# Performance work log

Measured on AMD Instinct MI355X. Metric: run time of the kernel, lower is better.

Reference implementation:

```python
import jax, jax.numpy as jnp
import numpy as np

B, D, N, M, R, C = 512, 16, 64, 32, 32, 10  # batch, divisions, feat_in, feat_map, TR-rank, categories


def setup_inputs() -> dict:
    key = jax.random.key(0)
    k1, k2, k3, k4 = jax.random.split(key, 4)
    tensor = jax.random.normal(k1, (B, D, N), dtype=jnp.float32)
    W_fm = jax.random.normal(k2, (N, M), dtype=jnp.float32) / np.sqrt(N)
    b_fm = jax.random.normal(k3, (M,), dtype=jnp.float32) * 0.01
    # one [R, M, R] tensor-ring core per (category, division)
    G = jax.random.normal(k4, (C, D, R, M, R), dtype=jnp.float32) / np.sqrt(M * R)
    return {"tensor": tensor, "W_fm": W_fm, "b_fm": b_fm, "G": G}


def reference(tensor, W_fm, b_fm, G):
    # FeatureMap: learned linear n -> m applied per division  [B, D, M]
    feat = jnp.einsum('bdn,nm->bdm', tensor, W_fm) + b_fm
    # CoreKernelTensorRing per (category, division): [B,M] x [R,M,R] -> [B,R,R]
    cores = jnp.einsum('bdm,cdimj->cdbij', feat, G)  # [C, D, B, R, R]
    # __foward_products: chained batched matmul along divisions (structural loop, D fixed)
    prod = cores[:, 0]  # [C, B, R, R]
    for d in range(1, D):
        prod = jnp.matmul(prod, cores[:, d])
    # __calculate_traces: per-sample trace, one logit per category
    logits = jnp.einsum('cbii->bc', prod)  # [B, C]
    return jax.nn.log_softmax(logits, axis=1)
```

## Files before the change

kernel.cpp:

```cpp
#include <hip/hip_runtime.h>
#include <math.h>

#define BB 512
#define DD 16
#define NN 64
#define MM 32
#define RR 32
#define CC 10
#define BBLK 16
#define SS 2
#define DSEG (DD / SS)
#define ROWH 40
#define BREGH 1304

typedef _Float16 v8h __attribute__((ext_vector_type(8)));
typedef float v4f __attribute__((ext_vector_type(4)));

union H8 { unsigned int u[4]; v8h h; _Float16 e[8]; };
union H4 { unsigned int u[2]; _Float16 e[4]; };

__device__ __forceinline__ unsigned int split_pack(float x) {
    _Float16 h = (_Float16)x;
    _Float16 l = (_Float16)(x - (float)h);
    unsigned int hb = (unsigned int)__builtin_bit_cast(unsigned short, h);
    unsigned int lb = (unsigned int)__builtin_bit_cast(unsigned short, l);
    return (hb << 16) | lb;
}

__device__ __forceinline__ float unpackf(unsigned int u) {
    _Float16 h = __builtin_bit_cast(_Float16, (unsigned short)(u >> 16));
    _Float16 l = __builtin_bit_cast(_Float16, (unsigned short)(u & 0xffffu));
    return (float)h + (float)l;
}

__global__ void produce_kernel(const float* __restrict__ tensor,
                               const float* __restrict__ W,
                               const float* __restrict__ bias,
                               const float* __restrict__ G,
                               _Float16* __restrict__ fh,
                               _Float16* __restrict__ gh) {
    if (blockIdx.x < 1024) {
        int t  = blockIdx.x * 256 + threadIdx.x;
        int m  = t & (MM - 1);
        int bd = t >> 5;
        const float* tp = tensor + bd * NN;
        float acc = bias[m];
#pragma unroll
        for (int n = 0; n < NN; ++n) acc += tp[n] * W[n * MM + m];
        fh[t] = (_Float16)acc;
    } else {
        int gid  = (blockIdx.x - 1024) * 256 + threadIdx.x;
        int l    = gid & 63;
        int tile = (gid >> 6) & 63;
        int d    = (gid >> 12) & 15;
        int c    = gid >> 16;
        int i    = tile >> 1;
        int jj   = 16 * (tile & 1) + (l & 15);
        int q    = l >> 4;
        const float* src = G + ((((size_t)c * DD + d) * RR + i) * MM + 8 * q) * RR + jj;
        H8 v;
#pragma unroll
        for (int r = 0; r < 8; ++r)
            v.e[r] = (_Float16)src[(size_t)r * RR];
        *(v8h*)(gh + (size_t)gid * 8) = v.h;
    }
}

__global__ __launch_bounds__(512, 6) void chain_kernel(
    const _Float16* __restrict__ feat_h,
    const _Float16* __restrict__ g_h,
    unsigned int* __restrict__ segP)
{
    __shared__ __align__(16) _Float16 lds[BBLK * BREGH];

    const int bid  = blockIdx.x;
    const int c    = bid >> 6;
    const int rem  = bid & 63;
    const int s    = rem & 1;
    const int b0   = (rem >> 1) * BBLK;
    const int d0   = s * DSEG;
    const int t    = threadIdx.x;
    const int w    = t >> 6;
    const int lane = t & 63;
    const int q    = lane >> 4;
    const int j4   = lane & 15;

    v8h pah[2][2];

    for (int dd = 0; dd < DSEG; ++dd) {
        const int d = d0 + dd;
        __syncthreads();
        {
            const size_t fo = (size_t)(b0 + j4) * (DD * MM) + d * MM + q * 8;
            v8h afh = *(const v8h*)(feat_h + fo);
            const size_t gbase = (size_t)(c * DD + d) * 32768;
#pragma unroll
            for (int jh = 0; jh < 2; ++jh) {
                v4f av[4];
#pragma unroll
                for (int ii = 0; ii < 4; ++ii) {
                    const int tile = w * 8 + 2 * ii + jh;
                    v8h g = *(const v8h*)(g_h + gbase + ((size_t)tile * 64 + lane) * 8);
                    v4f z = {0.f, 0.f, 0.f, 0.f};
                    av[ii] = __builtin_amdgcn_mfma_f32_16x16x32_f16(afh, g, z, 0, 0, 0);
                }
#pragma unroll
                for (int reg = 0; reg < 4; ++reg) {
                    H4 hv;
                    hv.e[0] = (_Float16)av[0][reg];
                    hv.e[1] = (_Float16)av[1][reg];
                    hv.e[2] = (_Float16)av[2][reg];
                    hv.e[3] = (_Float16)av[3][reg];
                    *reinterpret_cast<uint2*>(
                        &lds[(4 * q + reg) * BREGH + (16 * jh + j4) * ROWH + 4 * w]) =
                        make_uint2(hv.u[0], hv.u[1]);
                }
            }
        }
        __syncthreads();
#pragma unroll
        for (int cc = 0; cc < 2; ++cc) {
            const int b = 2 * w + cc;
            _Float16* base = lds + b * BREGH;
            if (dd == 0) {
#pragma unroll
                for (int mi = 0; mi < 2; ++mi) {
                    H8 a;
#pragma unroll
                    for (int r = 0; r < 8; ++r)
                        a.e[r] = base[(8 * q + r) * ROWH + 16 * mi + j4];
                    pah[cc][mi] = a.h;
                }
            } else {
                v8h bf[2];
#pragma unroll
                for (int ni = 0; ni < 2; ++ni)
                    bf[ni] = *(const v8h*)(base + (16 * ni + j4) * ROWH + 8 * q);
                v4f acc[2][2];
#pragma unroll
                for (int mi = 0; mi < 2; ++mi)
#pragma unroll
                    for (int ni = 0; ni < 2; ++ni) {
                        v4f z = {0.f, 0.f, 0.f, 0.f};
                        acc[mi][ni] = __builtin_amdgcn_mfma_f32_16x16x32_f16(
                            pah[cc][mi], bf[ni], z, 0, 0, 0);
                    }
                if (dd < DSEG - 1) {
#pragma unroll
                    for (int mi = 0; mi < 2; ++mi)
#pragma unroll
                        for (int ni = 0; ni < 2; ++ni)
#pragma unroll
                            for (int reg = 0; reg < 4; ++reg)
                                base[(16 * mi + 4 * q + reg) * ROWH + 16 * ni + j4] =
                                    (_Float16)acc[mi][ni][reg];
                    __builtin_amdgcn_sched_barrier(0);
#pragma unroll
                    for (int mi = 0; mi < 2; ++mi)
                        pah[cc][mi] = *(const v8h*)(base + (16 * mi + j4) * ROWH + 8 * q);
                } else {
                    unsigned int* dst = segP +
                        ((size_t)(c * BB + (b0 + b)) * SS + s) * 1024;
#pragma unroll
                    for (int mi = 0; mi < 2; ++mi)
#pragma unroll
                        for (int ni = 0; ni < 2; ++ni)
#pragma unroll
                            for (int reg = 0; reg < 4; ++reg)
                                dst[(16 * mi + 4 * q + reg) * 32 + 16 * ni + j4] =
                                    split_pack(acc[mi][ni][reg]);
                }
            }
        }
    }
}

__global__ __launch_bounds__(256) void combine_lsm_kernel(
    const unsigned int* __restrict__ segP,
    float* __restrict__ out)
{
    const int t    = threadIdx.x;
    const int b    = blockIdx.x * 4 + (t >> 6);
    const int lane = t & 63;
    const int i    = lane & 31;
    const int hf   = lane >> 5;

    float tr[CC];
#pragma unroll
    for (int c = 0; c < CC; ++c) {
        const unsigned int* P0 = segP + ((size_t)(c * BB + b) * SS + 0) * 1024;
        const unsigned int* P1 = P0 + 1024;
        const uint4* r0 = (const uint4*)(P0 + i * 32 + hf * 16);
        float acc = 0.f;
#pragma unroll
        for (int v = 0; v < 4; ++v) {
            uint4 x = r0[v];
            unsigned int us[4] = {x.x, x.y, x.z, x.w};
#pragma unroll
            for (int e = 0; e < 4; ++e) {
                int l = hf * 16 + v * 4 + e;
                acc += unpackf(us[e]) * unpackf(P1[l * 32 + i]);
            }
        }
        tr[c] = acc;
    }
#pragma unroll
    for (int c = 0; c < CC; ++c) {
#pragma unroll
        for (int off = 32; off > 0; off >>= 1)
            tr[c] += __shfl_down(tr[c], off);
    }
    if (lane == 0) {
        float mx = -1e30f;
#pragma unroll
        for (int c = 0; c < CC; ++c) mx = fmaxf(mx, tr[c]);
        float ssum = 0.f;
#pragma unroll
        for (int c = 0; c < CC; ++c) ssum += expf(tr[c] - mx);
        float ls = logf(ssum);
#pragma unroll
        for (int c = 0; c < CC; ++c) out[b * CC + c] = tr[c] - mx - ls;
    }
}

extern "C" void kernel_launch(void* const* d_in, const int* in_sizes, int n_in,
                              void* d_out, int out_size, void* d_ws, size_t ws_size,
                              hipStream_t stream) {
    const float* tensor = (const float*)d_in[0];
    const float* W      = (const float*)d_in[1];
    const float* bias   = (const float*)d_in[2];
    const float* G      = (const float*)d_in[3];
    float* out = (float*)d_out;

    const size_t FEAT = (size_t)BB * DD * MM;
    const size_t GPK  = (size_t)CC * DD * 64 * 64 * 8;
    _Float16* fh = (_Float16*)d_ws;
    _Float16* gh = fh + FEAT;
    unsigned int* segP = (unsigned int*)(gh + GPK);

    produce_kernel<<<1024 + (int)(GPK / 8 / 256), 256, 0, stream>>>(
        tensor, W, bias, G, fh, gh);
    chain_kernel<<<CC * (BB / BBLK) * SS, 512, 0, stream>>>(fh, gh, segP);
    combine_lsm_kernel<<<BB / 4, 256, 0, stream>>>(segP, out);
}
```

Measured before the change: 135.1 us.

## Run full 16-division chain per block with 8 samples, drop segment-combine split

Removes the two-segment split of the division chain: each block now processes 8 samples across all 16 divisions, computes the trace in-register with a wave shuffle, and writes logits directly, followed by a tiny log-softmax kernel. Core weights for the next division are prefetched into registers while the current one is consumed, and half of the MFMA core outputs are redundant (only q<2 lanes store). This eliminates the split/pack intermediate buffer and the combine kernel's global traffic. In exchange it halves per-block sample reuse of G loads and lengthens the serial dependency chain per block, so there are fewer, longer blocks (640 vs 1280).

```diff
diff --git a/kernel.cpp b/kernel.cpp
--- a/kernel.cpp
+++ b/kernel.cpp
@@ -7,9 +7,7 @@
 #define MM 32
 #define RR 32
 #define CC 10
-#define BBLK 16
-#define SS 2
-#define DSEG (DD / SS)
+#define BBLK 8
 #define ROWH 40
 #define BREGH 1304
 
@@ -18,20 +16,6 @@
 
 union H8 { unsigned int u[4]; v8h h; _Float16 e[8]; };
 union H4 { unsigned int u[2]; _Float16 e[4]; };
-
-__device__ __forceinline__ unsigned int split_pack(float x) {
-    _Float16 h = (_Float16)x;
-    _Float16 l = (_Float16)(x - (float)h);
-    unsigned int hb = (unsigned int)__builtin_bit_cast(unsigned short, h);
-    unsigned int lb = (unsigned int)__builtin_bit_cast(unsigned short, l);
-    return (hb << 16) | lb;
-}
-
-__device__ __forceinline__ float unpackf(unsigned int u) {
-    _Float16 h = __builtin_bit_cast(_Float16, (unsigned short)(u >> 16));
-    _Float16 l = __builtin_bit_cast(_Float16, (unsigned short)(u & 0xffffu));
-    return (float)h + (float)l;
-}
 
 __global__ void produce_kernel(const float* __restrict__ tensor,
                                const float* __restrict__ W,
@@ -66,161 +50,133 @@
     }
 }
 
-__global__ __launch_bounds__(512, 6) void chain_kernel(
+__global__ __launch_bounds__(512, 4) void chain_kernel(
     const _Float16* __restrict__ feat_h,
     const _Float16* __restrict__ g_h,
-    unsigned int* __restrict__ segP)
+    float* __restrict__ logits)
 {
     __shared__ __align__(16) _Float16 lds[BBLK * BREGH];
 
     const int bid  = blockIdx.x;
     const int c    = bid >> 6;
-    const int rem  = bid & 63;
-    const int s    = rem & 1;
-    const int b0   = (rem >> 1) * BBLK;
-    const int d0   = s * DSEG;
+    const int b0   = (bid & 63) * BBLK;
     const int t    = threadIdx.x;
     const int w    = t >> 6;
     const int lane = t & 63;
     const int q    = lane >> 4;
     const int j4   = lane & 15;
 
-    v8h pah[2][2];
-
-    for (int dd = 0; dd < DSEG; ++dd) {
-        const int d = d0 + dd;
+    const size_t gbase_c = (size_t)c * DD * 32768;
+    const int bA = b0 + (j4 & 7);
+
+    v8h afh = *(const v8h*)(feat_h + (size_t)bA * (DD * MM) + 0 * MM + q * 8);
+    v8h gf[8];
+#pragma unroll
+    for (int u = 0; u < 8; ++u) {
+        const int tile = w * 8 + u;
+        gf[u] = *(const v8h*)(g_h + gbase_c + ((size_t)tile * 64 + lane) * 8);
+    }
+
+    v8h pah[2];
+    v4f acc[2][2];
+
+    for (int d = 0; d < DD; ++d) {
         __syncthreads();
-        {
-            const size_t fo = (size_t)(b0 + j4) * (DD * MM) + d * MM + q * 8;
-            v8h afh = *(const v8h*)(feat_h + fo);
-            const size_t gbase = (size_t)(c * DD + d) * 32768;
-#pragma unroll
-            for (int jh = 0; jh < 2; ++jh) {
-                v4f av[4];
-#pragma unroll
-                for (int ii = 0; ii < 4; ++ii) {
-                    const int tile = w * 8 + 2 * ii + jh;
-                    v8h g = *(const v8h*)(g_h + gbase + ((size_t)tile * 64 + lane) * 8);
-                    v4f z = {0.f, 0.f, 0.f, 0.f};
-                    av[ii] = __builtin_amdgcn_mfma_f32_16x16x32_f16(afh, g, z, 0, 0, 0);
-                }
+        v4f av[8];
+#pragma unroll
+        for (int u = 0; u < 8; ++u) {
+            v4f z = {0.f, 0.f, 0.f, 0.f};
+            av[u] = __builtin_amdgcn_mfma_f32_16x16x32_f16(afh, gf[u], z, 0, 0, 0);
+        }
+        if (d < DD - 1) {
+            afh = *(const v8h*)(feat_h + (size_t)bA * (DD * MM) + (d + 1) * MM + q * 8);
+            const size_t gb = gbase_c + (size_t)(d + 1) * 32768;
+#pragma unroll
+            for (int u = 0; u < 8; ++u) {
+                const int tile = w * 8 + u;
+                gf[u] = *(const v8h*)(g_h + gb + ((size_t)tile * 64 + lane) * 8);
+            }
+        }
+        if (q < 2) {
+#pragma unroll
+            for (int jh = 0; jh < 2; ++jh)
 #pragma unroll
                 for (int reg = 0; reg < 4; ++reg) {
                     H4 hv;
-                    hv.e[0] = (_Float16)av[0][reg];
-                    hv.e[1] = (_Float16)av[1][reg];
-                    hv.e[2] = (_Float16)av[2][reg];
-                    hv.e[3] = (_Float16)av[3][reg];
+                    hv.e[0] = (_Float16)av[0 * 2 + jh][reg];
+                    hv.e[1] = (_Float16)av[1 * 2 + jh][reg];
+                    hv.e[2] = (_Float16)av[2 * 2 + jh][reg];
+                    hv.e[3] = (_Float16)av[3 * 2 + jh][reg];
                     *reinterpret_cast<uint2*>(
                         &lds[(4 * q + reg) * BREGH + (16 * jh + j4) * ROWH + 4 * w]) =
                         make_uint2(hv.u[0], hv.u[1]);
                 }
+        }
+        __syncthreads();
+        _Float16* base = lds + w * BREGH;
+        if (d == 0) {
+#pragma unroll
+            for (int mi = 0; mi < 2; ++mi) {
+                H8 a;
+#pragma unroll
+                for (int r = 0; r < 8; ++r)
+                    a.e[r] = base[(8 * q + r) * ROWH + 16 * mi + j4];
+                pah[mi] = a.h;
             }
-        }
-        __syncthreads();
-#pragma unroll
-        for (int cc = 0; cc < 2; ++cc) {
-            const int b = 2 * w + cc;
-            _Float16* base = lds + b * BREGH;
-            if (dd == 0) {
-#pragma unroll
-                for (int mi = 0; mi < 2; ++mi) {
-                    H8 a;
-#pragma unroll
-                    for (int r = 0; r < 8; ++r)
-                        a.e[r] = base[(8 * q + r) * ROWH + 16 * mi + j4];
-                    pah[cc][mi] = a.h;
+        } else {
+            v8h bf[2];
+#pragma unroll
+            for (int ni = 0; ni < 2; ++ni)
+                bf[ni] = *(const v8h*)(base + (16 * ni + j4) * ROWH + 8 * q);
+#pragma unroll
+            for (int mi = 0; mi < 2; ++mi)
+#pragma unroll
+                for (int ni = 0; ni < 2; ++ni) {
+                    v4f z = {0.f, 0.f, 0.f, 0.f};
+                    acc[mi][ni] = __builtin_amdgcn_mfma_f32_16x16x32_f16(
+                        pah[mi], bf[ni], z, 0, 0, 0);
                 }
-            } else {
-                v8h bf[2];
-#pragma unroll
-                for (int ni = 0; ni < 2; ++ni)
-                    bf[ni] = *(const v8h*)(base + (16 * ni + j4) * ROWH + 8 * q);
-                v4f acc[2][2];
+            if (d < DD - 1) {
 #pragma unroll
                 for (int mi = 0; mi < 2; ++mi)
 #pragma unroll
-                    for (int ni = 0; ni < 2; ++ni) {
-                        v4f z = {0.f, 0.f, 0.f, 0.f};
-                        acc[mi][ni] = __builtin_amdgcn_mfma_f32_16x16x32_f16(
-                            pah[cc][mi], bf[ni], z, 0, 0, 0);
-                    }
-                if (dd < DSEG - 1) {
-#pragma unroll
-                    for (int mi = 0; mi < 2; ++mi)
-#pragma unroll
-                        for (int ni = 0; ni < 2; ++ni)
-#pragma unroll
-                            for (int reg = 0; reg < 4; ++reg)
-                                base[(16 * mi + 4 * q + reg) * ROWH + 16 * ni + j4] =
-                                    (_Float16)acc[mi][ni][reg];
-                    __builtin_amdgcn_sched_barrier(0);
-#pragma unroll
-                    for (int mi = 0; mi < 2; ++mi)
-                        pah[cc][mi] = *(const v8h*)(base + (16 * mi + j4) * ROWH + 8 * q);
-                } else {
-                    unsigned int* dst = segP +
-                        ((size_t)(c * BB + (b0 + b)) * SS + s) * 1024;
-#pragma unroll
-                    for (int mi = 0; mi < 2; ++mi)
-#pragma unroll
-                        for (int ni = 0; ni < 2; ++ni)
-#pragma unroll
-                            for (int reg = 0; reg < 4; ++reg)
-                                dst[(16 * mi + 4 * q + reg) * 32 + 16 * ni + j4] =
-                                    split_pack(acc[mi][ni][reg]);
-                }
+                    for (int ni = 0; ni < 2; ++ni)
+#pragma unroll
+                        for (int reg = 0; reg < 4; ++reg)
+                            base[(16 * mi + 4 * q + reg) * ROWH + 16 * ni + j4] =
+                                (_Float16)acc[mi][ni][reg];
+                __builtin_amdgcn_sched_barrier(0);
+#pragma unroll
+                for (int mi = 0; mi < 2; ++mi)
+                    pah[mi] = *(const v8h*)(base + (16 * mi + j4) * ROWH + 8 * q);
             }
         }
     }
-}
-
-__global__ __launch_bounds__(256) void combine_lsm_kernel(
-    const unsigned int* __restrict__ segP,
-    float* __restrict__ out)
-{
-    const int t    = threadIdx.x;
-    const int b    = blockIdx.x * 4 + (t >> 6);
-    const int lane = t & 63;
-    const int i    = lane & 31;
-    const int hf   = lane >> 5;
-
-    float tr[CC];
-#pragma unroll
-    for (int c = 0; c < CC; ++c) {
-        const unsigned int* P0 = segP + ((size_t)(c * BB + b) * SS + 0) * 1024;
-        const unsigned int* P1 = P0 + 1024;
-        const uint4* r0 = (const uint4*)(P0 + i * 32 + hf * 16);
-        float acc = 0.f;
-#pragma unroll
-        for (int v = 0; v < 4; ++v) {
-            uint4 x = r0[v];
-            unsigned int us[4] = {x.x, x.y, x.z, x.w};
-#pragma unroll
-            for (int e = 0; e < 4; ++e) {
-                int l = hf * 16 + v * 4 + e;
-                acc += unpackf(us[e]) * unpackf(P1[l * 32 + i]);
-            }
-        }
-        tr[c] = acc;
-    }
-#pragma unroll
-    for (int c = 0; c < CC; ++c) {
-#pragma unroll
-        for (int off = 32; off > 0; off >>= 1)
-            tr[c] += __shfl_down(tr[c], off);
-    }
-    if (lane == 0) {
-        float mx = -1e30f;
-#pragma unroll
-        for (int c = 0; c < CC; ++c) mx = fmaxf(mx, tr[c]);
-        float ssum = 0.f;
-#pragma unroll
-        for (int c = 0; c < CC; ++c) ssum += expf(tr[c] - mx);
-        float ls = logf(ssum);
-#pragma unroll
-        for (int c = 0; c < CC; ++c) out[b * CC + c] = tr[c] - mx - ls;
-    }
+
+    float tr = 0.f;
+    if (q == (j4 >> 2)) {
+        int reg = j4 & 3;
+        tr = acc[0][0][reg] + acc[1][1][reg];
+    }
+#pragma unroll
+    for (int off = 32; off > 0; off >>= 1) tr += __shfl_down(tr, off);
+    if (lane == 0) logits[(b0 + w) * CC + c] = tr;
+}
+
+__global__ void lsm_kernel(const float* __restrict__ logits,
+                           float* __restrict__ out) {
+    int b = blockIdx.x * blockDim.x + threadIdx.x;
+    if (b >= BB) return;
+    float x[CC];
+    float mx = -1e30f;
+#pragma unroll
+    for (int c = 0; c < CC; ++c) { x[c] = logits[b * CC + c]; mx = fmaxf(mx, x[c]); }
+    float s = 0.f;
+#pragma unroll
+    for (int c = 0; c < CC; ++c) s += expf(x[c] - mx);
+    float ls = logf(s);
+#pragma unroll
+    for (int c = 0; c < CC; ++c) out[b * CC + c] = x[c] - mx - ls;
 }
 
 extern "C" void kernel_launch(void* const* d_in, const int* in_sizes, int n_in,
@@ -236,10 +192,10 @@
     const size_t GPK  = (size_t)CC * DD * 64 * 64 * 8;
     _Float16* fh = (_Float16*)d_ws;
     _Float16* gh = fh + FEAT;
-    unsigned int* segP = (unsigned int*)(gh + GPK);
+    float* logits = (float*)(gh + GPK);
 
     produce_kernel<<<1024 + (int)(GPK / 8 / 256), 256, 0, stream>>>(
         tensor, W, bias, G, fh, gh);
-    chain_kernel<<<CC * (BB / BBLK) * SS, 512, 0, stream>>>(fh, gh, segP);
-    combine_lsm_kernel<<<BB / 4, 256, 0, stream>>>(segP, out);
-}
+    chain_kernel<<<CC * (BB / BBLK), 512, 0, stream>>>(fh, gh, logits);
+    lsm_kernel<<<(BB + 255) / 256, 256, 0, stream>>>(logits, out);
+}
```

After: 125.1 us. 7.5% less time.
